# Kernel optimization log

Hardware: AMD Instinct MI355X
Metric: run time of the kernel (lower is better)

## Reference

```python
import jax, jax.numpy as jnp
import numpy as np

NEG_SLOPE = 0.01  # torch LeakyReLU default

def setup_inputs() -> dict:
    key = jax.random.key(0)
    ks = jax.random.split(key, 16)
    B, T = 256, 168
    LAG, LAT, WS, H = 168, 128, 64, 1024
    def lin(kw, kb, out_f, in_f):
        bound = 1.0 / np.sqrt(in_f)
        W = jax.random.uniform(kw, (out_f, in_f), jnp.float32, -bound, bound)
        b = jax.random.uniform(kb, (out_f,), jnp.float32, -bound, bound)
        return W, b
    W1, b1 = lin(ks[0], ks[1], 64, LAG)
    W2, b2 = lin(ks[2], ks[3], LAT, 64)
    W3, b3 = lin(ks[4], ks[5], H, LAT)
    bound = 1.0 / np.sqrt(H)
    Wih = jax.random.uniform(ks[6], (3 * H, WS), jnp.float32, -bound, bound)
    Whh = jax.random.uniform(ks[7], (3 * H, H), jnp.float32, -bound, bound)
    bih = jax.random.uniform(ks[8], (3 * H,), jnp.float32, -bound, bound)
    bhh = jax.random.uniform(ks[9], (3 * H,), jnp.float32, -bound, bound)
    Wo, bo = lin(ks[10], ks[11], 1, H)
    lag = jax.random.normal(ks[12], (B, LAG), jnp.float32)
    curr = jax.random.normal(ks[13], (T, B, WS), jnp.float32)
    return dict(lag=lag, curr=curr, W1=W1, b1=b1, W2=W2, b2=b2, W3=W3, b3=b3,
                Wih=Wih, Whh=Whh, bih=bih, bhh=bhh, Wo=Wo, bo=bo)

def _leaky(x):
    return jnp.where(x >= 0, x, NEG_SLOPE * x)

def reference(lag, curr, W1, b1, W2, b2, W3, b3, Wih, Whh, bih, bhh, Wo, bo):
    # Encoder MLP: lag -> 64 -> latent -> hidden (leaky relu after first two)
    h = _leaky(lag @ W1.T + b1)
    h = _leaky(h @ W2.T + b2)
    h0 = h @ W3.T + b3  # [B, H]
    H = h0.shape[-1]

    def step(h_t, x_t):
        gi = x_t @ Wih.T + bih          # [B, 3H]
        gh = h_t @ Whh.T + bhh          # [B, 3H]
        ir, iz, inn = jnp.split(gi, 3, axis=-1)
        hr, hz, hn = jnp.split(gh, 3, axis=-1)
        r = jax.nn.sigmoid(ir + hr)
        z = jax.nn.sigmoid(iz + hz)
        n = jnp.tanh(inn + r * hn)
        h_new = (1.0 - z) * n + z * h_t
        return h_new, h_new

    _, hs = jax.lax.scan(step, h0, curr)          # hs: [T, B, H]
    preds = jnp.squeeze(hs @ Wo.T + bo, -1)       # [T, B]
    return preds.T                                 # [B, T]
```

## Files before the change

kernel.cpp:

```cpp
#include <hip/hip_runtime.h>
#include <hip/hip_bf16.h>
#include <cstdint>
#include <cstddef>

typedef _Float16 half8 __attribute__((ext_vector_type(8)));
typedef _Float16 half4 __attribute__((ext_vector_type(4)));
typedef float floatx4 __attribute__((ext_vector_type(4)));
typedef unsigned long long u64;

#define B_ 256
#define T_ 168
#define H_ 1024
#define WS_ 64
#define LAG_ 168
#define LAT_ 128

__device__ __forceinline__ float fast_sigmoid(float x) {
    return __builtin_amdgcn_rcpf(1.f + __expf(-x));
}
__device__ __forceinline__ float fast_tanh(float x) {
    return 1.f - 2.f * __builtin_amdgcn_rcpf(__expf(2.f * x) + 1.f);
}

__global__ void cvt_all(const float4* __restrict__ a, half4* __restrict__ da, int na,
                        const float4* __restrict__ b, half4* __restrict__ db, int nb,
                        const float4* __restrict__ c, half4* __restrict__ dc, int nc) {
    int i = blockIdx.x * blockDim.x + threadIdx.x;
    const float4* s;
    half4* d;
    int j = i;
    if (j < na) { s = a; d = da; }
    else {
        j -= na;
        if (j < nb) { s = b; d = db; }
        else {
            j -= nb;
            if (j >= nc) return;
            s = c; d = dc;
        }
    }
    float4 v = s[j];
    half4 o;
    o[0] = (_Float16)v.x; o[1] = (_Float16)v.y;
    o[2] = (_Float16)v.z; o[3] = (_Float16)v.w;
    d[j] = o;
}

__global__ void enc12(const float* __restrict__ in, const float* __restrict__ W,
                      const float* __restrict__ bias, float* __restrict__ outb, int infeat) {
    int r = blockIdx.x, j = threadIdx.x;
    const float* row = in + (size_t)r * infeat;
    const float* w   = W  + (size_t)j * infeat;
    float s = bias[j];
    for (int k = 0; k < infeat; ++k) s += row[k] * w[k];
    outb[(size_t)r * blockDim.x + j] = (s >= 0.f) ? s : 0.01f * s;
}

__global__ void enc3(const float* __restrict__ h2, const float* __restrict__ W3,
                     const float* __restrict__ b3, float* __restrict__ hprev32,
                     _Float16* __restrict__ h0f16) {
    __shared__ float s[LAT_];
    int r = blockIdx.x;
    if (threadIdx.x < LAT_) s[threadIdx.x] = h2[(size_t)r * LAT_ + threadIdx.x];
    __syncthreads();
    for (int j = threadIdx.x; j < H_; j += 256) {
        const float* w = W3 + (size_t)j * LAT_;
        float acc = b3[j];
        #pragma unroll 8
        for (int k = 0; k < LAT_; ++k) acc += s[k] * w[k];
        hprev32[(size_t)r * H_ + j] = acc;
        h0f16[(size_t)r * H_ + j]   = (_Float16)acc;
    }
}

__global__ __launch_bounds__(256, 1) void gru_persistent(
    _Float16* __restrict__ hbuf,
    const float* __restrict__ hprev32, const _Float16* __restrict__ whh16,
    const _Float16* __restrict__ wih16, const _Float16* __restrict__ x16,
    const float* __restrict__ bih, const float* __restrict__ bhh,
    const float* __restrict__ Wo, float* __restrict__ partials,
    unsigned* __restrict__ bar)
{
    __shared__ __align__(16) _Float16 Ash[16 * 1032];
    __shared__ __align__(16) _Float16 Wsh[192 * 72];
    __shared__ __align__(16) _Float16 Hsh[4 * 256];

    const int tid  = threadIdx.x;
    const int w    = tid >> 6;
    const int lane = tid & 63;
    const int m16  = lane & 15;
    const int quad = lane >> 4;
    const int pi   = blockIdx.x & 15;
    const int qi   = blockIdx.x >> 4;
    const int pi16 = pi << 4;
    const int u    = (qi << 6) + (w << 4) + m16;

    for (int idx = tid; idx < 1536; idx += 256) {
        int rowl = idx >> 3, ch = idx & 7;
        int g = rowl >> 6, ru = rowl & 63;
        *(uint4*)(&Wsh[rowl * 72 + (ch << 3)]) =
            *(const uint4*)(wih16 + (size_t)(((g << 10) + (qi << 6) + ru) << 6) + (ch << 3));
    }

    half8 br[32], bz[32];
    {
        const _Float16* p0 = whh16 + ((size_t)u << 10) + (quad << 3);
        const _Float16* p1 = whh16 + ((size_t)(H_ + u) << 10) + (quad << 3);
        #pragma unroll
        for (int c = 0; c < 32; ++c) br[c] = *(const half8*)(p0 + (c << 5));
        #pragma unroll
        for (int c = 0; c < 32; ++c) bz[c] = *(const half8*)(p1 + (c << 5));
    }
    const _Float16* bnp = whh16 + ((size_t)(2 * H_ + u) << 10) + (quad << 3);

    const float b_r  = bih[u]          + bhh[u];
    const float b_z  = bih[H_ + u]     + bhh[H_ + u];
    const float b_in = bih[2 * H_ + u];
    const float b_hn = bhh[2 * H_ + u];
    const float wo_u = Wo[u];

    float hreg[4];
    #pragma unroll
    for (int i = 0; i < 4; ++i)
        hreg[i] = hprev32[((size_t)(pi16 + (quad << 2) + i) << 10) + u];

    __syncthreads();

    unsigned* flag_self       = bar + (((pi << 4) | qi) << 4);
    const unsigned* flag_peer = bar + (((pi << 4) | (lane & 15)) << 4);
    const int srow = tid >> 4;
    const int sch  = tid & 15;
    const int prow = lane >> 2;
    const int pc4  = lane & 3;

    for (int t = 0; t < T_; ++t) {
        const _Float16* hsrc = hbuf + (size_t)(t & 3) * (B_ * H_);
        _Float16*       hdst = hbuf + (size_t)((t + 1) & 3) * (B_ * H_);

        half8 ax0 = *(const half8*)(x16 + (((size_t)t << 8) + pi16 + m16) * WS_ + (quad << 3));
        half8 ax1 = *(const half8*)(x16 + (((size_t)t << 8) + pi16 + m16) * WS_ + 32 + (quad << 3));
        half8 bnA[8], bnB[8];
        #pragma unroll
        for (int j = 0; j < 8; ++j) bnA[j] = *(const half8*)(bnp + (j << 5));

        const unsigned need = (unsigned)t;
        u64 rdy = 0;

        while ((rdy & 0xFull) != 0xFull) {
            unsigned f = 0;
            if (lane < 16)
                f = __hip_atomic_load(flag_peer, __ATOMIC_RELAXED, __HIP_MEMORY_SCOPE_AGENT);
            rdy |= __ballot(f >= need);
            if ((rdy & 0xFull) != 0xFull) __builtin_amdgcn_s_sleep(1);
        }
        u64 va0, va1, va2, va3;
        {
            const _Float16* s = hsrc + ((size_t)(pi16 + srow) << 10) + (sch << 4);
            va0 = __hip_atomic_load((const u64*)(s + 0),  __ATOMIC_RELAXED, __HIP_MEMORY_SCOPE_AGENT);
            va1 = __hip_atomic_load((const u64*)(s + 4),  __ATOMIC_RELAXED, __HIP_MEMORY_SCOPE_AGENT);
            va2 = __hip_atomic_load((const u64*)(s + 8),  __ATOMIC_RELAXED, __HIP_MEMORY_SCOPE_AGENT);
            va3 = __hip_atomic_load((const u64*)(s + 12), __ATOMIC_RELAXED, __HIP_MEMORY_SCOPE_AGENT);
        }

        floatx4 acc_r  = {b_r,  b_r,  b_r,  b_r };
        floatx4 acc_z  = {b_z,  b_z,  b_z,  b_z };
        floatx4 acc_in = {b_in, b_in, b_in, b_in};
        floatx4 acc_hn = {b_hn, b_hn, b_hn, b_hn};

        {
            half8 p0 = *(const half8*)(&Wsh[((w << 4) + m16) * 72        + (quad << 3)]);
            half8 p1 = *(const half8*)(&Wsh[(64 + (w << 4) + m16) * 72   + (quad << 3)]);
            half8 p2 = *(const half8*)(&Wsh[(128 + (w << 4) + m16) * 72  + (quad << 3)]);
            acc_r  = __builtin_amdgcn_mfma_f32_16x16x32_f16(ax0, p0, acc_r,  0, 0, 0);
            acc_z  = __builtin_amdgcn_mfma_f32_16x16x32_f16(ax0, p1, acc_z,  0, 0, 0);
            acc_in = __builtin_amdgcn_mfma_f32_16x16x32_f16(ax0, p2, acc_in, 0, 0, 0);
            half8 q0 = *(const half8*)(&Wsh[((w << 4) + m16) * 72        + 32 + (quad << 3)]);
            half8 q1 = *(const half8*)(&Wsh[(64 + (w << 4) + m16) * 72   + 32 + (quad << 3)]);
            half8 q2 = *(const half8*)(&Wsh[(128 + (w << 4) + m16) * 72  + 32 + (quad << 3)]);
            acc_r  = __builtin_amdgcn_mfma_f32_16x16x32_f16(ax1, q0, acc_r,  0, 0, 0);
            acc_z  = __builtin_amdgcn_mfma_f32_16x16x32_f16(ax1, q1, acc_z,  0, 0, 0);
            acc_in = __builtin_amdgcn_mfma_f32_16x16x32_f16(ax1, q2, acc_in, 0, 0, 0);
        }

        #pragma unroll
        for (int g = 0; g < 4; ++g) {
            {
                _Float16* d = &Ash[srow * 1032 + (g << 8) + (sch << 4)];
                *(u64*)(d + 0)  = va0;
                *(u64*)(d + 4)  = va1;
                *(u64*)(d + 8)  = va2;
                *(u64*)(d + 12) = va3;
            }
            __syncthreads();
            if (g < 3) {
                const u64 mask = 0xFull << ((g + 1) << 2);
                while ((rdy & mask) != mask) {
                    unsigned f = 0;
                    if (lane < 16)
                        f = __hip_atomic_load(flag_peer, __ATOMIC_RELAXED, __HIP_MEMORY_SCOPE_AGENT);
                    rdy |= __ballot(f >= need);
                    if ((rdy & mask) != mask) __builtin_amdgcn_s_sleep(1);
                }
                const _Float16* s = hsrc + ((size_t)(pi16 + srow) << 10) + ((g + 1) << 8) + (sch << 4);
                va0 = __hip_atomic_load((const u64*)(s + 0),  __ATOMIC_RELAXED, __HIP_MEMORY_SCOPE_AGENT);
                va1 = __hip_atomic_load((const u64*)(s + 4),  __ATOMIC_RELAXED, __HIP_MEMORY_SCOPE_AGENT);
                va2 = __hip_atomic_load((const u64*)(s + 8),  __ATOMIC_RELAXED, __HIP_MEMORY_SCOPE_AGENT);
                va3 = __hip_atomic_load((const u64*)(s + 12), __ATOMIC_RELAXED, __HIP_MEMORY_SCOPE_AGENT);
                #pragma unroll
                for (int j = 0; j < 8; ++j)
                    bnB[j] = *(const half8*)(bnp + ((((g + 1) << 3) + j) << 5));
            }
            #pragma unroll
            for (int j = 0; j < 8; ++j) {
                const int c = (g << 3) + j;
                half8 a = *(const half8*)(&Ash[m16 * 1032 + (c << 5) + (quad << 3)]);
                acc_r  = __builtin_amdgcn_mfma_f32_16x16x32_f16(a, br[c], acc_r,  0, 0, 0);
                acc_z  = __builtin_amdgcn_mfma_f32_16x16x32_f16(a, bz[c], acc_z,  0, 0, 0);
                acc_hn = __builtin_amdgcn_mfma_f32_16x16x32_f16(a, bnA[j], acc_hn, 0, 0, 0);
            }
            if (g < 3) {
                #pragma unroll
                for (int j = 0; j < 8; ++j) bnA[j] = bnB[j];
            }
        }

        float pv[4];
        #pragma unroll
        for (int i = 0; i < 4; ++i) {
            float rg = fast_sigmoid(acc_r[i]);
            float zg = fast_sigmoid(acc_z[i]);
            float ng = fast_tanh(acc_in[i] + rg * acc_hn[i]);
            float hn2 = (1.f - zg) * ng + zg * hreg[i];
            hreg[i] = hn2;
            pv[i] = hn2 * wo_u;
            Hsh[(w << 8) + ((quad << 2) + i) * 16 + m16] = (_Float16)hn2;
        }
        __threadfence_block();
        {
            u64 hv = *(const u64*)(&Hsh[(w << 8) + prow * 16 + (pc4 << 2)]);
            __hip_atomic_store(
                (u64*)(hdst + ((size_t)(pi16 + prow) << 10) + (qi << 6) + (w << 4) + (pc4 << 2)),
                hv, __ATOMIC_RELAXED, __HIP_MEMORY_SCOPE_AGENT);
        }
        #pragma unroll
        for (int m = 1; m < 16; m <<= 1) {
            #pragma unroll
            for (int i = 0; i < 4; ++i) pv[i] += __shfl_xor(pv[i], m);
        }
        asm volatile("s_waitcnt vmcnt(0)" ::: "memory");
        __syncthreads();
        if (tid == 0)
            __hip_atomic_store(flag_self, (unsigned)(t + 1),
                               __ATOMIC_RELAXED, __HIP_MEMORY_SCOPE_AGENT);
        if (m16 == 0) {
            #pragma unroll
            for (int i = 0; i < 4; ++i)
                partials[((size_t)t * B_ + pi16 + (quad << 2) + i) * 64 + (qi << 2) + w] = pv[i];
        }
    }
}

__global__ void out_reduce(const float* __restrict__ partials, const float* __restrict__ bo,
                           float* __restrict__ out) {
    int t = blockIdx.x, r = threadIdx.x;
    const float* p = partials + ((size_t)t * B_ + r) * 64;
    float s = 0.f;
    #pragma unroll
    for (int i = 0; i < 64; ++i) s += p[i];
    out[(size_t)r * T_ + t] = s + bo[0];
}

extern "C" void kernel_launch(void* const* d_in, const int* in_sizes, int n_in,
                              void* d_out, int out_size, void* d_ws, size_t ws_size,
                              hipStream_t stream) {
    const float* lag  = (const float*)d_in[0];
    const float* curr = (const float*)d_in[1];
    const float* W1   = (const float*)d_in[2];
    const float* b1   = (const float*)d_in[3];
    const float* W2   = (const float*)d_in[4];
    const float* b2   = (const float*)d_in[5];
    const float* W3   = (const float*)d_in[6];
    const float* b3   = (const float*)d_in[7];
    const float* Wih  = (const float*)d_in[8];
    const float* Whh  = (const float*)d_in[9];
    const float* bih  = (const float*)d_in[10];
    const float* bhh  = (const float*)d_in[11];
    const float* Wo   = (const float*)d_in[12];
    const float* bo   = (const float*)d_in[13];
    float* out = (float*)d_out;

    char* ws = (char*)d_ws;
    size_t off = 0;
    auto alloc = [&](size_t bytes) -> void* {
        void* p = ws + off;
        off += (bytes + 255) & ~(size_t)255;
        return p;
    };
    _Float16* whh16 = (_Float16*)alloc((size_t)3 * H_ * H_ * 2);
    _Float16* wih16 = (_Float16*)alloc((size_t)3 * H_ * WS_ * 2);
    _Float16* x16   = (_Float16*)alloc((size_t)T_ * B_ * WS_ * 2);
    _Float16* hbuf  = (_Float16*)alloc((size_t)4 * B_ * H_ * 2);
    float* hprev32  = (float*)alloc((size_t)B_ * H_ * 4);
    float* h1       = (float*)alloc((size_t)B_ * 64 * 4);
    float* h2       = (float*)alloc((size_t)B_ * LAT_ * 4);
    float* partials = (float*)alloc((size_t)T_ * B_ * 64 * 4);
    unsigned* bar   = (unsigned*)alloc(81920);

    hipMemsetAsync(bar, 0, 81920, stream);

    const int na = 3 * H_ * H_ / 4;
    const int nb = 3 * H_ * WS_ / 4;
    const int nc = T_ * B_ * WS_ / 4;
    const int ntot = na + nb + nc;
    cvt_all<<<(ntot + 255) / 256, 256, 0, stream>>>(
        (const float4*)Whh, (half4*)whh16, na,
        (const float4*)Wih, (half4*)wih16, nb,
        (const float4*)curr, (half4*)x16, nc);

    enc12<<<B_, 64, 0, stream>>>(lag, W1, b1, h1, LAG_);
    enc12<<<B_, LAT_, 0, stream>>>(h1, W2, b2, h2, 64);
    enc3<<<B_, 256, 0, stream>>>(h2, W3, b3, hprev32, hbuf);

    gru_persistent<<<dim3(256), dim3(256), 0, stream>>>(
        hbuf, hprev32, whh16, wih16, x16, bih, bhh, Wo, partials, bar);

    out_reduce<<<T_, B_, 0, stream>>>(partials, bo, out);
}
```

Measured before the change: 808.2 us.

## Keep all Whh gates in registers, fuse encoder, drop staged h pipeline

Keeps the full n-gate Whh slice resident in registers alongside the r and z slices, so the per-step global reloads of the n-gate weights go away. Replaces the four-stage wait, load and compute pipeline over h chunks with a single wait for all peers, one bulk load and one sync. Also fuses the three encoder kernels into one, and transposes the partials layout so the output reduction reads coalesced. The extra register use (96 half8 weight vectors per thread) risks spills, and dropping the staged overlap can expose more barrier latency each step.

Result: slower. 876.7 us (+8.5%).

```diff
diff --git a/kernel.cpp b/kernel.cpp
--- a/kernel.cpp
+++ b/kernel.cpp
@@ -46,28 +46,36 @@
     d[j] = o;
 }
 
-__global__ void enc12(const float* __restrict__ in, const float* __restrict__ W,
-                      const float* __restrict__ bias, float* __restrict__ outb, int infeat) {
-    int r = blockIdx.x, j = threadIdx.x;
-    const float* row = in + (size_t)r * infeat;
-    const float* w   = W  + (size_t)j * infeat;
-    float s = bias[j];
-    for (int k = 0; k < infeat; ++k) s += row[k] * w[k];
-    outb[(size_t)r * blockDim.x + j] = (s >= 0.f) ? s : 0.01f * s;
-}
-
-__global__ void enc3(const float* __restrict__ h2, const float* __restrict__ W3,
-                     const float* __restrict__ b3, float* __restrict__ hprev32,
-                     _Float16* __restrict__ h0f16) {
-    __shared__ float s[LAT_];
-    int r = blockIdx.x;
-    if (threadIdx.x < LAT_) s[threadIdx.x] = h2[(size_t)r * LAT_ + threadIdx.x];
+__global__ void enc_fused(const float* __restrict__ lag,
+                          const float* __restrict__ W1, const float* __restrict__ b1,
+                          const float* __restrict__ W2, const float* __restrict__ b2,
+                          const float* __restrict__ W3, const float* __restrict__ b3,
+                          float* __restrict__ hprev32, _Float16* __restrict__ h0f16) {
+    __shared__ float lrow[LAG_];
+    __shared__ float l1[64];
+    __shared__ float l2[LAT_];
+    const int r = blockIdx.x, tid = threadIdx.x;
+    if (tid < LAG_) lrow[tid] = lag[(size_t)r * LAG_ + tid];
     __syncthreads();
-    for (int j = threadIdx.x; j < H_; j += 256) {
+    if (tid < 64) {
+        const float* w = W1 + (size_t)tid * LAG_;
+        float s = b1[tid];
+        for (int k = 0; k < LAG_; ++k) s += lrow[k] * w[k];
+        l1[tid] = (s >= 0.f) ? s : 0.01f * s;
+    }
+    __syncthreads();
+    if (tid < LAT_) {
+        const float* w = W2 + (size_t)tid * 64;
+        float s = b2[tid];
+        for (int k = 0; k < 64; ++k) s += l1[k] * w[k];
+        l2[tid] = (s >= 0.f) ? s : 0.01f * s;
+    }
+    __syncthreads();
+    for (int j = tid; j < H_; j += 256) {
         const float* w = W3 + (size_t)j * LAT_;
         float acc = b3[j];
         #pragma unroll 8
-        for (int k = 0; k < LAT_; ++k) acc += s[k] * w[k];
+        for (int k = 0; k < LAT_; ++k) acc += l2[k] * w[k];
         hprev32[(size_t)r * H_ + j] = acc;
         h0f16[(size_t)r * H_ + j]   = (_Float16)acc;
     }
@@ -102,16 +110,18 @@
             *(const uint4*)(wih16 + (size_t)(((g << 10) + (qi << 6) + ru) << 6) + (ch << 3));
     }
 
-    half8 br[32], bz[32];
+    half8 br[32], bz[32], bn[32];
     {
         const _Float16* p0 = whh16 + ((size_t)u << 10) + (quad << 3);
         const _Float16* p1 = whh16 + ((size_t)(H_ + u) << 10) + (quad << 3);
+        const _Float16* p2 = whh16 + ((size_t)(2 * H_ + u) << 10) + (quad << 3);
         #pragma unroll
         for (int c = 0; c < 32; ++c) br[c] = *(const half8*)(p0 + (c << 5));
         #pragma unroll
         for (int c = 0; c < 32; ++c) bz[c] = *(const half8*)(p1 + (c << 5));
-    }
-    const _Float16* bnp = whh16 + ((size_t)(2 * H_ + u) << 10) + (quad << 3);
+        #pragma unroll
+        for (int c = 0; c < 32; ++c) bn[c] = *(const half8*)(p2 + (c << 5));
+    }
 
     const float b_r  = bih[u]          + bhh[u];
     const float b_z  = bih[H_ + u]     + bhh[H_ + u];
@@ -139,27 +149,28 @@
 
         half8 ax0 = *(const half8*)(x16 + (((size_t)t << 8) + pi16 + m16) * WS_ + (quad << 3));
         half8 ax1 = *(const half8*)(x16 + (((size_t)t << 8) + pi16 + m16) * WS_ + 32 + (quad << 3));
-        half8 bnA[8], bnB[8];
-        #pragma unroll
-        for (int j = 0; j < 8; ++j) bnA[j] = *(const half8*)(bnp + (j << 5));
 
         const unsigned need = (unsigned)t;
         u64 rdy = 0;
 
-        while ((rdy & 0xFull) != 0xFull) {
+        while ((rdy & 0xFFFFull) != 0xFFFFull) {
             unsigned f = 0;
             if (lane < 16)
                 f = __hip_atomic_load(flag_peer, __ATOMIC_RELAXED, __HIP_MEMORY_SCOPE_AGENT);
             rdy |= __ballot(f >= need);
-            if ((rdy & 0xFull) != 0xFull) __builtin_amdgcn_s_sleep(1);
-        }
-        u64 va0, va1, va2, va3;
+            if ((rdy & 0xFFFFull) != 0xFFFFull) __builtin_amdgcn_s_sleep(1);
+        }
+
+        u64 va[4][4];
         {
             const _Float16* s = hsrc + ((size_t)(pi16 + srow) << 10) + (sch << 4);
-            va0 = __hip_atomic_load((const u64*)(s + 0),  __ATOMIC_RELAXED, __HIP_MEMORY_SCOPE_AGENT);
-            va1 = __hip_atomic_load((const u64*)(s + 4),  __ATOMIC_RELAXED, __HIP_MEMORY_SCOPE_AGENT);
-            va2 = __hip_atomic_load((const u64*)(s + 8),  __ATOMIC_RELAXED, __HIP_MEMORY_SCOPE_AGENT);
-            va3 = __hip_atomic_load((const u64*)(s + 12), __ATOMIC_RELAXED, __HIP_MEMORY_SCOPE_AGENT);
+            #pragma unroll
+            for (int g = 0; g < 4; ++g) {
+                #pragma unroll
+                for (int k = 0; k < 4; ++k)
+                    va[g][k] = __hip_atomic_load((const u64*)(s + (g << 8) + (k << 2)),
+                                                 __ATOMIC_RELAXED, __HIP_MEMORY_SCOPE_AGENT);
+            }
         }
 
         floatx4 acc_r  = {b_r,  b_r,  b_r,  b_r };
@@ -182,46 +193,25 @@
             acc_in = __builtin_amdgcn_mfma_f32_16x16x32_f16(ax1, q2, acc_in, 0, 0, 0);
         }
 
-        #pragma unroll
-        for (int g = 0; g < 4; ++g) {
-            {
-                _Float16* d = &Ash[srow * 1032 + (g << 8) + (sch << 4)];
-                *(u64*)(d + 0)  = va0;
-                *(u64*)(d + 4)  = va1;
-                *(u64*)(d + 8)  = va2;
-                *(u64*)(d + 12) = va3;
+        {
+            _Float16* dbase = &Ash[srow * 1032 + (sch << 4)];
+            #pragma unroll
+            for (int g = 0; g < 4; ++g) {
+                _Float16* d = dbase + (g << 8);
+                *(u64*)(d + 0)  = va[g][0];
+                *(u64*)(d + 4)  = va[g][1];
+                *(u64*)(d + 8)  = va[g][2];
+                *(u64*)(d + 12) = va[g][3];
             }
-            __syncthreads();
-            if (g < 3) {
-                const u64 mask = 0xFull << ((g + 1) << 2);
-                while ((rdy & mask) != mask) {
-                    unsigned f = 0;
-                    if (lane < 16)
-                        f = __hip_atomic_load(flag_peer, __ATOMIC_RELAXED, __HIP_MEMORY_SCOPE_AGENT);
-                    rdy |= __ballot(f >= need);
-                    if ((rdy & mask) != mask) __builtin_amdgcn_s_sleep(1);
-                }
-                const _Float16* s = hsrc + ((size_t)(pi16 + srow) << 10) + ((g + 1) << 8) + (sch << 4);
-                va0 = __hip_atomic_load((const u64*)(s + 0),  __ATOMIC_RELAXED, __HIP_MEMORY_SCOPE_AGENT);
-                va1 = __hip_atomic_load((const u64*)(s + 4),  __ATOMIC_RELAXED, __HIP_MEMORY_SCOPE_AGENT);
-                va2 = __hip_atomic_load((const u64*)(s + 8),  __ATOMIC_RELAXED, __HIP_MEMORY_SCOPE_AGENT);
-                va3 = __hip_atomic_load((const u64*)(s + 12), __ATOMIC_RELAXED, __HIP_MEMORY_SCOPE_AGENT);
-                #pragma unroll
-                for (int j = 0; j < 8; ++j)
-                    bnB[j] = *(const half8*)(bnp + ((((g + 1) << 3) + j) << 5));
-            }
-            #pragma unroll
-            for (int j = 0; j < 8; ++j) {
-                const int c = (g << 3) + j;
-                half8 a = *(const half8*)(&Ash[m16 * 1032 + (c << 5) + (quad << 3)]);
-                acc_r  = __builtin_amdgcn_mfma_f32_16x16x32_f16(a, br[c], acc_r,  0, 0, 0);
-                acc_z  = __builtin_amdgcn_mfma_f32_16x16x32_f16(a, bz[c], acc_z,  0, 0, 0);
-                acc_hn = __builtin_amdgcn_mfma_f32_16x16x32_f16(a, bnA[j], acc_hn, 0, 0, 0);
-            }
-            if (g < 3) {
-                #pragma unroll
-                for (int j = 0; j < 8; ++j) bnA[j] = bnB[j];
-            }
+        }
+        __syncthreads();
+
+        #pragma unroll
+        for (int c = 0; c < 32; ++c) {
+            half8 a = *(const half8*)(&Ash[m16 * 1032 + (c << 5) + (quad << 3)]);
+            acc_r  = __builtin_amdgcn_mfma_f32_16x16x32_f16(a, br[c], acc_r,  0, 0, 0);
+            acc_z  = __builtin_amdgcn_mfma_f32_16x16x32_f16(a, bz[c], acc_z,  0, 0, 0);
+            acc_hn = __builtin_amdgcn_mfma_f32_16x16x32_f16(a, bn[c], acc_hn, 0, 0, 0);
         }
 
         float pv[4];
@@ -255,7 +245,7 @@
         if (m16 == 0) {
             #pragma unroll
             for (int i = 0; i < 4; ++i)
-                partials[((size_t)t * B_ + pi16 + (quad << 2) + i) * 64 + (qi << 2) + w] = pv[i];
+                partials[((size_t)(t << 6) + (qi << 2) + w) * 256 + pi16 + (quad << 2) + i] = pv[i];
         }
     }
 }
@@ -263,10 +253,9 @@
 __global__ void out_reduce(const float* __restrict__ partials, const float* __restrict__ bo,
                            float* __restrict__ out) {
     int t = blockIdx.x, r = threadIdx.x;
-    const float* p = partials + ((size_t)t * B_ + r) * 64;
     float s = 0.f;
     #pragma unroll
-    for (int i = 0; i < 64; ++i) s += p[i];
+    for (int k = 0; k < 64; ++k) s += partials[((size_t)(t << 6) + k) * 256 + r];
     out[(size_t)r * T_ + t] = s + bo[0];
 }
 
@@ -301,8 +290,6 @@
     _Float16* x16   = (_Float16*)alloc((size_t)T_ * B_ * WS_ * 2);
     _Float16* hbuf  = (_Float16*)alloc((size_t)4 * B_ * H_ * 2);
     float* hprev32  = (float*)alloc((size_t)B_ * H_ * 4);
-    float* h1       = (float*)alloc((size_t)B_ * 64 * 4);
-    float* h2       = (float*)alloc((size_t)B_ * LAT_ * 4);
     float* partials = (float*)alloc((size_t)T_ * B_ * 64 * 4);
     unsigned* bar   = (unsigned*)alloc(81920);
 
@@ -317,9 +304,7 @@
         (const float4*)Wih, (half4*)wih16, nb,
         (const float4*)curr, (half4*)x16, nc);
 
-    enc12<<<B_, 64, 0, stream>>>(lag, W1, b1, h1, LAG_);
-    enc12<<<B_, LAT_, 0, stream>>>(h1, W2, b2, h2, 64);
-    enc3<<<B_, 256, 0, stream>>>(h2, W3, b3, hprev32, hbuf);
+    enc_fused<<<B_, 256, 0, stream>>>(lag, W1, b1, W2, b2, W3, b3, hprev32, hbuf);
 
     gru_persistent<<<dim3(256), dim3(256), 0, stream>>>(
         hbuf, hprev32, whh16, wih16, x16, bih, bhh, Wo, partials, bar);
```
